# Kernel tuning notes

Hardware: AMD Instinct MI355X
Metric: run time of the kernel (lower is better)

The kernel has to match this reference:

```python
import jax, jax.numpy as jnp
import numpy as np

COMMITMENT_COST = 0.25


def setup_inputs() -> dict:
    key = jax.random.key(0)
    k1, k2 = jax.random.split(key)
    B, C, H, W, D = 8, 64, 32, 32, 32
    NUM_EMB = 512
    x = jax.random.normal(k1, (B, C, H, W, D), dtype=jnp.float32)
    # torch init: uniform(-1/num_embeddings, 1/num_embeddings)
    codebook = jax.random.uniform(k2, (NUM_EMB, C), dtype=jnp.float32,
                                  minval=-1.0 / NUM_EMB, maxval=1.0 / NUM_EMB)
    return {"x": x, "codebook": codebook}


def reference(x, codebook):
    B, C, H, W, D = x.shape
    # [B,C,H,W,D] -> [N, C] with N = B*H*W*D
    flat = jnp.transpose(x, (0, 2, 3, 4, 1)).reshape(-1, C)
    # squared L2 distances to every codebook entry: [N, num_embeddings]
    dist = (jnp.sum(flat * flat, axis=1, keepdims=True)
            - 2.0 * flat @ codebook.T
            + jnp.sum(codebook * codebook, axis=1))
    idx = jnp.argmin(dist, axis=1)                     # [N]
    # one-hot @ codebook  ==  gather (same math, efficient form)
    quant_flat = codebook[idx]                          # [N, C]
    quant = jnp.transpose(quant_flat.reshape(B, H, W, D, C), (0, 4, 1, 2, 3))
    e_loss = jnp.mean((jax.lax.stop_gradient(quant) - x) ** 2)
    q_loss = jnp.mean((quant - jax.lax.stop_gradient(x)) ** 2)
    loss = q_loss + COMMITMENT_COST * e_loss
    # straight-through estimator
    quant_st = x + jax.lax.stop_gradient(quant - x)
    return quant_st, loss
```

## Files before the change

kernel.cpp:

```cpp
#include <hip/hip_runtime.h>
#include <cstdint>
#include <cstddef>

#define SPATIAL   32768
#define CHANNELS  64
#define NUM_EMB   512
#define NPOS      262144
#define OUT_ELEMS 16777216
#define BLOCK     256
#define LOSS_SCALE (1.25f / 16777216.0f)

typedef __attribute__((ext_vector_type(8))) short bf16x8;
typedef __attribute__((ext_vector_type(4))) float f32x4;

union b8u { int i[4]; bf16x8 v; };
union fiu { float f; unsigned u; };

__device__ __forceinline__ short f2bf_rne(float f) {
    fiu v; v.f = f;
    unsigned r = v.u + 0x7fffu + ((v.u >> 16) & 1u);
    return (short)(r >> 16);
}

__global__ void vq_prep(const float* __restrict__ cb,
                        short* __restrict__ cbfrag,
                        float* __restrict__ cbn,
                        float* __restrict__ loss_slot) {
    int e = blockIdx.x * blockDim.x + threadIdx.x;
    if (e == 0) *loss_slot = 0.0f;
    if (e < NUM_EMB) {
        const int nt  = e >> 4;
        const int col = e & 15;
        float s = 0.0f;
#pragma unroll
        for (int q = 0; q < 4; ++q) {
#pragma unroll
            for (int j = 0; j < 8; ++j) {
                float v0 = cb[e * CHANNELS + q * 8 + j];
                float v1 = cb[e * CHANNELS + 32 + q * 8 + j];
                cbfrag[nt * 1024 + (q * 16 + col) * 8 + j]       = f2bf_rne(v0);
                cbfrag[nt * 1024 + 512 + (q * 16 + col) * 8 + j] = f2bf_rne(v1);
            }
        }
#pragma unroll
        for (int c = 0; c < CHANNELS; ++c) {
            float v = cb[e * CHANNELS + c];
            s = __builtin_fmaf(v, v, s);
        }
        cbn[e] = -0.5f * s;
    }
}

__global__ __launch_bounds__(BLOCK) void vq_main(
    const float* __restrict__ x,
    const float* __restrict__ cb,
    const short* __restrict__ cbfrag,
    const float* __restrict__ cbn,
    float* __restrict__ out,
    float* __restrict__ loss_slot) {
#pragma clang fp contract(off)
    __shared__ int   cand[BLOCK];
    __shared__ float wsum[4];

    const int tid  = threadIdx.x;
    const int wave = tid >> 6, lane = tid & 63;
    const int q    = lane >> 4, col = lane & 15;

    const int blockPos = blockIdx.x * BLOCK;
    const int b     = blockPos >> 15;
    const int sbase = blockPos & 32767;
    const float* xb = x + (size_t)b * (CHANNELS * SPATIAL);
    const int wbase = sbase + wave * 64;

    b8u A[4][2];
#pragma unroll
    for (int t = 0; t < 4; ++t) {
        const unsigned* pu = (const unsigned*)xb + (wbase + t * 16 + col);
#pragma unroll
        for (int kh = 0; kh < 2; ++kh) {
#pragma unroll
            for (int jj = 0; jj < 4; ++jj) {
                unsigned u0 = pu[(size_t)(kh * 32 + q * 8 + 2 * jj + 0) * SPATIAL];
                unsigned u1 = pu[(size_t)(kh * 32 + q * 8 + 2 * jj + 1) * SPATIAL];
                A[t][kh].i[jj] = __builtin_amdgcn_perm(u1, u0, 0x07060302u);
            }
        }
    }

    float m[4][4];
#pragma unroll
    for (int t = 0; t < 4; ++t)
#pragma unroll
        for (int r = 0; r < 4; ++r) m[t][r] = -3.4e38f;

    const unsigned MASK = 0xFFFFFE00u;
    const int encBase = 511 - col;

    for (int nt = 0; nt < 32; ++nt) {
        const int e0 = nt * 16;
        const short* fbase = cbfrag + nt * 1024 + lane * 8;
        bf16x8 B0 = *(const bf16x8*)(fbase);
        bf16x8 B1 = *(const bf16x8*)(fbase + 512);
        float cn = cbn[e0 + col];
        f32x4 ci = {cn, cn, cn, cn};
        const unsigned enc = (unsigned)(encBase - e0);
#pragma unroll
        for (int t = 0; t < 4; ++t) {
            f32x4 acc = __builtin_amdgcn_mfma_f32_16x16x32_bf16(A[t][0].v, B0, ci, 0, 0, 0);
            acc = __builtin_amdgcn_mfma_f32_16x16x32_bf16(A[t][1].v, B1, acc, 0, 0, 0);
#pragma unroll
            for (int r = 0; r < 4; ++r) {
                fiu p; p.f = acc[r];
                p.u = (p.u & MASK) | enc;
                m[t][r] = fmaxf(m[t][r], p.f);
            }
        }
    }

#pragma unroll
    for (int t = 0; t < 4; ++t) {
#pragma unroll
        for (int r = 0; r < 4; ++r) {
            float v = m[t][r];
#pragma unroll
            for (int d = 1; d < 16; d <<= 1)
                v = fmaxf(v, __shfl_xor(v, d, 64));
            if (col == 0) {
                fiu p; p.f = v;
                cand[wave * 64 + t * 16 + q * 4 + r] = 511 - (int)(p.u & 511u);
            }
        }
    }

    const int bidx = cand[tid];
    const f32x4* qv = (const f32x4*)(cb + (size_t)bidx * CHANNELS);
    const float* px = xb + (sbase + tid);
    float* op = out + (size_t)b * (CHANNELS * SPATIAL) + (sbase + tid);
    float lsum = 0.0f;
#pragma unroll
    for (int c4 = 0; c4 < 16; ++c4) {
        f32x4 qq = qv[c4];
#pragma unroll
        for (int j = 0; j < 4; ++j) {
            const int c = c4 * 4 + j;
            float xv = px[(size_t)c * SPATIAL];
            float t2 = qq[j] - xv;
            op[(size_t)c * SPATIAL] = xv + t2;
            lsum = __builtin_fmaf(t2, t2, lsum);
        }
    }

#pragma unroll
    for (int off = 32; off > 0; off >>= 1) lsum += __shfl_down(lsum, off, 64);
    if (lane == 0) wsum[wave] = lsum;
    __syncthreads();
    if (tid == 0) {
        float bs = (wsum[0] + wsum[1]) + (wsum[2] + wsum[3]);
        atomicAdd(loss_slot, bs * LOSS_SCALE);
    }
}

extern "C" void kernel_launch(void* const* d_in, const int* in_sizes, int n_in,
                              void* d_out, int out_size, void* d_ws, size_t ws_size,
                              hipStream_t stream) {
    const float* x  = (const float*)d_in[0];
    const float* cb = (const float*)d_in[1];
    float* out = (float*)d_out;
    short* cbfrag = (short*)d_ws;
    float* cbn    = (float*)(cbfrag + NUM_EMB * CHANNELS);
    float* loss_slot = out + OUT_ELEMS;

    vq_prep<<<2, 256, 0, stream>>>(cb, cbfrag, cbn, loss_slot);
    vq_main<<<NPOS / BLOCK, BLOCK, 0, stream>>>(x, cb, cbfrag, cbn, out, loss_slot);
}
```

Before: 149.2 us.

## Stage codebook fragments in LDS with double-buffered async loads and coalesced gather

The bf16 codebook fragments are now loaded into shared memory in four chunks using global_load_lds, double-buffered so the next chunk streams in while MFMAs run on the current one. The epilogue gather of selected codebook rows is restaged through a swizzled LDS buffer with coalesced row loads, in two halves of 32 channels. This is meant to cut per-wave global/L2 traffic for codebook reads and make the gather coalesced. The cost is 32KB of LDS per block, which may lower occupancy, plus extra barriers.

```diff
diff --git a/kernel.cpp b/kernel.cpp
--- a/kernel.cpp
+++ b/kernel.cpp
@@ -9,6 +9,11 @@
 #define OUT_ELEMS 16777216
 #define BLOCK     256
 #define LOSS_SCALE (1.25f / 16777216.0f)
+
+#define NT_TOTAL     32
+#define NT_PER_CHUNK 8
+#define NCHUNK       4
+#define CHUNK_BYTES  16384
 
 typedef __attribute__((ext_vector_type(8))) short bf16x8;
 typedef __attribute__((ext_vector_type(4))) float f32x4;
@@ -59,8 +64,12 @@
     float* __restrict__ out,
     float* __restrict__ loss_slot) {
 #pragma clang fp contract(off)
+    __shared__ __align__(16) char smem[32768];
     __shared__ int   cand[BLOCK];
     __shared__ float wsum[4];
+
+    short* stageS = (short*)smem;
+    float* qbuf   = (float*)smem;
 
     const int tid  = threadIdx.x;
     const int wave = tid >> 6, lane = tid & 63;
@@ -72,6 +81,18 @@
     const float* xb = x + (size_t)b * (CHANNELS * SPATIAL);
     const int wbase = sbase + wave * 64;
 
+    {
+#pragma unroll
+        for (int rd = 0; rd < 4; ++rd) {
+            const int off = rd * 4096 + wave * 1024;
+            const unsigned* g = (const unsigned*)((const char*)cbfrag + off + lane * 16);
+            unsigned* l = (unsigned*)(smem + off);
+            __builtin_amdgcn_global_load_lds(
+                (const __attribute__((address_space(1))) unsigned*)g,
+                (__attribute__((address_space(3))) unsigned*)l, 16, 0, 0);
+        }
+    }
+
     b8u A[4][2];
 #pragma unroll
     for (int t = 0; t < 4; ++t) {
@@ -96,25 +117,46 @@
     const unsigned MASK = 0xFFFFFE00u;
     const int encBase = 511 - col;
 
-    for (int nt = 0; nt < 32; ++nt) {
-        const int e0 = nt * 16;
-        const short* fbase = cbfrag + nt * 1024 + lane * 8;
-        bf16x8 B0 = *(const bf16x8*)(fbase);
-        bf16x8 B1 = *(const bf16x8*)(fbase + 512);
-        float cn = cbn[e0 + col];
-        f32x4 ci = {cn, cn, cn, cn};
-        const unsigned enc = (unsigned)(encBase - e0);
-#pragma unroll
-        for (int t = 0; t < 4; ++t) {
-            f32x4 acc = __builtin_amdgcn_mfma_f32_16x16x32_bf16(A[t][0].v, B0, ci, 0, 0, 0);
-            acc = __builtin_amdgcn_mfma_f32_16x16x32_bf16(A[t][1].v, B1, acc, 0, 0, 0);
-#pragma unroll
-            for (int r = 0; r < 4; ++r) {
-                fiu p; p.f = acc[r];
-                p.u = (p.u & MASK) | enc;
-                m[t][r] = fmaxf(m[t][r], p.f);
-            }
-        }
+    __syncthreads();
+
+#pragma unroll 1
+    for (int c = 0; c < NCHUNK; ++c) {
+        const int buf = c & 1;
+        if (c + 1 < NCHUNK) {
+#pragma unroll
+            for (int rd = 0; rd < 4; ++rd) {
+                const int off = rd * 4096 + wave * 1024;
+                const unsigned* g = (const unsigned*)
+                    ((const char*)cbfrag + (c + 1) * CHUNK_BYTES + off + lane * 16);
+                unsigned* l = (unsigned*)(smem + (buf ^ 1) * CHUNK_BYTES + off);
+                __builtin_amdgcn_global_load_lds(
+                    (const __attribute__((address_space(1))) unsigned*)g,
+                    (__attribute__((address_space(3))) unsigned*)l, 16, 0, 0);
+            }
+        }
+#pragma unroll
+        for (int k = 0; k < NT_PER_CHUNK; ++k) {
+            const int nt = c * NT_PER_CHUNK + k;
+            const int e0 = nt * 16;
+            const short* sb = stageS + buf * (CHUNK_BYTES / 2) + k * 1024 + lane * 8;
+            bf16x8 B0 = *(const bf16x8*)sb;
+            bf16x8 B1 = *(const bf16x8*)(sb + 512);
+            float cn = cbn[e0 + col];
+            f32x4 ci = {cn, cn, cn, cn};
+            const unsigned enc = (unsigned)(encBase - e0);
+#pragma unroll
+            for (int t = 0; t < 4; ++t) {
+                f32x4 acc = __builtin_amdgcn_mfma_f32_16x16x32_bf16(A[t][0].v, B0, ci, 0, 0, 0);
+                acc = __builtin_amdgcn_mfma_f32_16x16x32_bf16(A[t][1].v, B1, acc, 0, 0, 0);
+#pragma unroll
+                for (int r = 0; r < 4; ++r) {
+                    fiu p; p.f = acc[r];
+                    p.u = (p.u & MASK) | enc;
+                    m[t][r] = fmaxf(m[t][r], p.f);
+                }
+            }
+        }
+        __syncthreads();
     }
 
 #pragma unroll
@@ -131,23 +173,42 @@
             }
         }
     }
-
-    const int bidx = cand[tid];
-    const f32x4* qv = (const f32x4*)(cb + (size_t)bidx * CHANNELS);
-    const float* px = xb + (sbase + tid);
-    float* op = out + (size_t)b * (CHANNELS * SPATIAL) + (sbase + tid);
+    __syncthreads();
+
+    const int pos = tid;
+    const int gr  = tid >> 3;
+    const int gl  = tid & 7;
+    const float* pxb = xb + (sbase + pos);
+    float* opb = out + (size_t)b * (CHANNELS * SPATIAL) + (sbase + pos);
     float lsum = 0.0f;
-#pragma unroll
-    for (int c4 = 0; c4 < 16; ++c4) {
-        f32x4 qq = qv[c4];
-#pragma unroll
-        for (int j = 0; j < 4; ++j) {
-            const int c = c4 * 4 + j;
-            float xv = px[(size_t)c * SPATIAL];
-            float t2 = qq[j] - xv;
-            op[(size_t)c * SPATIAL] = xv + t2;
-            lsum = __builtin_fmaf(t2, t2, lsum);
-        }
+
+#pragma unroll 1
+    for (int cc = 0; cc < 2; ++cc) {
+#pragma unroll
+        for (int rd = 0; rd < 8; ++rd) {
+            const int r   = rd * 32 + gr;
+            const int row = cand[r];
+            f32x4 v = *((const f32x4*)(cb + (size_t)row * CHANNELS + cc * 32) + gl);
+            const int lsw = gl ^ (r & 7);
+            *((f32x4*)(qbuf + r * 32 + lsw * 4)) = v;
+        }
+        __syncthreads();
+        const float* px = pxb + (size_t)(cc * 32) * SPATIAL;
+        float* op = opb + (size_t)(cc * 32) * SPATIAL;
+#pragma unroll
+        for (int j = 0; j < 8; ++j) {
+            const int jsw = j ^ (pos & 7);
+            f32x4 qq = *((const f32x4*)(qbuf + pos * 32 + jsw * 4));
+#pragma unroll
+            for (int k = 0; k < 4; ++k) {
+                const int ch = j * 4 + k;
+                float xv = px[(size_t)ch * SPATIAL];
+                float t2 = qq[k] - xv;
+                op[(size_t)ch * SPATIAL] = xv + t2;
+                lsum = __builtin_fmaf(t2, t2, lsum);
+            }
+        }
+        if (cc == 0) __syncthreads();
     }
 
 #pragma unroll
```

Measured after the change: 141.6 us. 1.05x faster.

## Stage codebook fragments in LDS with double-buffered async loads and halve positions per block

Applied to the files above, without the earlier changes.

Each block now handles 128 positions instead of 256 with the same 256 threads, and swaps the MFMA operand order so the codebook is the A operand. Codebook bf16 fragments are streamed into LDS through double-buffered global_load_lds copies instead of per-wave global loads. The output gather stages selected codebook rows in a swizzled LDS buffer so each thread reads vectors, and the loss/writeback loop is split across two thread halves. This is meant to cut register pressure (launch bounds raised to 6 blocks/CU) and repeated global codebook reads, at the cost of more __syncthreads and twice as many blocks.

```diff
diff --git a/kernel.cpp b/kernel.cpp
--- a/kernel.cpp
+++ b/kernel.cpp
@@ -8,6 +8,7 @@
 #define NPOS      262144
 #define OUT_ELEMS 16777216
 #define BLOCK     256
+#define POSB      128
 #define LOSS_SCALE (1.25f / 16777216.0f)
 
 typedef __attribute__((ext_vector_type(8))) short bf16x8;
@@ -51,7 +52,7 @@
     }
 }
 
-__global__ __launch_bounds__(BLOCK) void vq_main(
+__global__ __launch_bounds__(BLOCK, 6) void vq_main(
     const float* __restrict__ x,
     const float* __restrict__ cb,
     const short* __restrict__ cbfrag,
@@ -59,95 +60,136 @@
     float* __restrict__ out,
     float* __restrict__ loss_slot) {
 #pragma clang fp contract(off)
-    __shared__ int   cand[BLOCK];
+    __shared__ __align__(16) char arena[16384];
+    __shared__ int   cand[POSB];
     __shared__ float wsum[4];
+
+    short* stageS = (short*)arena;
+    float* qbuf   = (float*)arena;
 
     const int tid  = threadIdx.x;
     const int wave = tid >> 6, lane = tid & 63;
     const int q    = lane >> 4, col = lane & 15;
 
-    const int blockPos = blockIdx.x * BLOCK;
+    const int blockPos = blockIdx.x * POSB;
     const int b     = blockPos >> 15;
     const int sbase = blockPos & 32767;
     const float* xb = x + (size_t)b * (CHANNELS * SPATIAL);
-    const int wbase = sbase + wave * 64;
-
-    b8u A[4][2];
-#pragma unroll
-    for (int t = 0; t < 4; ++t) {
+    const int wbase = sbase + wave * 32;
+
+#pragma unroll
+    for (int rd = 0; rd < 2; ++rd) {
+        const int off = rd * 4096 + wave * 1024;
+        __builtin_amdgcn_global_load_lds(
+            (const __attribute__((address_space(1))) unsigned*)
+                ((const char*)cbfrag + off + lane * 16),
+            (__attribute__((address_space(3))) unsigned*)(arena + off), 16, 0, 0);
+    }
+    __builtin_amdgcn_sched_barrier(0);
+
+    b8u A[2][2];
+#pragma unroll
+    for (int t = 0; t < 2; ++t) {
         const unsigned* pu = (const unsigned*)xb + (wbase + t * 16 + col);
 #pragma unroll
-        for (int kh = 0; kh < 2; ++kh) {
+        for (int kh = 0; kh < 2; ++kh)
 #pragma unroll
             for (int jj = 0; jj < 4; ++jj) {
                 unsigned u0 = pu[(size_t)(kh * 32 + q * 8 + 2 * jj + 0) * SPATIAL];
                 unsigned u1 = pu[(size_t)(kh * 32 + q * 8 + 2 * jj + 1) * SPATIAL];
                 A[t][kh].i[jj] = __builtin_amdgcn_perm(u1, u0, 0x07060302u);
             }
-        }
-    }
-
-    float m[4][4];
-#pragma unroll
-    for (int t = 0; t < 4; ++t)
-#pragma unroll
-        for (int r = 0; r < 4; ++r) m[t][r] = -3.4e38f;
-
+    }
+
+    __syncthreads();
+
+    float mt[2];
+    mt[0] = -3.4e38f; mt[1] = -3.4e38f;
     const unsigned MASK = 0xFFFFFE00u;
-    const int encBase = 511 - col;
-
-    for (int nt = 0; nt < 32; ++nt) {
-        const int e0 = nt * 16;
-        const short* fbase = cbfrag + nt * 1024 + lane * 8;
-        bf16x8 B0 = *(const bf16x8*)(fbase);
-        bf16x8 B1 = *(const bf16x8*)(fbase + 512);
-        float cn = cbn[e0 + col];
-        f32x4 ci = {cn, cn, cn, cn};
-        const unsigned enc = (unsigned)(encBase - e0);
-#pragma unroll
-        for (int t = 0; t < 4; ++t) {
-            f32x4 acc = __builtin_amdgcn_mfma_f32_16x16x32_bf16(A[t][0].v, B0, ci, 0, 0, 0);
-            acc = __builtin_amdgcn_mfma_f32_16x16x32_bf16(A[t][1].v, B1, acc, 0, 0, 0);
-#pragma unroll
-            for (int r = 0; r < 4; ++r) {
-                fiu p; p.f = acc[r];
-                p.u = (p.u & MASK) | enc;
-                m[t][r] = fmaxf(m[t][r], p.f);
-            }
-        }
-    }
-
-#pragma unroll
-    for (int t = 0; t < 4; ++t) {
-#pragma unroll
-        for (int r = 0; r < 4; ++r) {
-            float v = m[t][r];
-#pragma unroll
-            for (int d = 1; d < 16; d <<= 1)
-                v = fmaxf(v, __shfl_xor(v, d, 64));
-            if (col == 0) {
-                fiu p; p.f = v;
-                cand[wave * 64 + t * 16 + q * 4 + r] = 511 - (int)(p.u & 511u);
-            }
-        }
-    }
-
-    const int bidx = cand[tid];
-    const f32x4* qv = (const f32x4*)(cb + (size_t)bidx * CHANNELS);
-    const float* px = xb + (sbase + tid);
-    float* op = out + (size_t)b * (CHANNELS * SPATIAL) + (sbase + tid);
+
+    int buf = 0;
+#pragma unroll 1
+    for (int c = 0; c < 8; ++c) {
+        if (c < 7) {
+#pragma unroll
+            for (int rd = 0; rd < 2; ++rd) {
+                const int off = rd * 4096 + wave * 1024;
+                __builtin_amdgcn_global_load_lds(
+                    (const __attribute__((address_space(1))) unsigned*)
+                        ((const char*)cbfrag + (c + 1) * 8192 + off + lane * 16),
+                    (__attribute__((address_space(3))) unsigned*)
+                        (arena + (buf ^ 1) * 8192 + off), 16, 0, 0);
+            }
+        }
+#pragma unroll
+        for (int k = 0; k < 4; ++k) {
+            const int nt = c * 4 + k;
+            const short* sb = stageS + buf * 4096 + k * 1024 + (lane << 3);
+            bf16x8 CB0 = *(const bf16x8*)sb;
+            bf16x8 CB1 = *(const bf16x8*)(sb + 512);
+            f32x4 civ  = *(const f32x4*)(cbn + nt * 16 + (q << 2));
+            const unsigned encq = (unsigned)(511 - nt * 16 - (q << 2));
+#pragma unroll
+            for (int tt = 0; tt < 2; ++tt) {
+                f32x4 acc = __builtin_amdgcn_mfma_f32_16x16x32_bf16(CB0, A[tt][0].v, civ, 0, 0, 0);
+                acc = __builtin_amdgcn_mfma_f32_16x16x32_bf16(CB1, A[tt][1].v, acc, 0, 0, 0);
+                fiu p0, p1, p2, p3;
+                p0.f = acc[0]; p0.u = (p0.u & MASK) | (encq - 0);
+                p1.f = acc[1]; p1.u = (p1.u & MASK) | (encq - 1);
+                p2.f = acc[2]; p2.u = (p2.u & MASK) | (encq - 2);
+                p3.f = acc[3]; p3.u = (p3.u & MASK) | (encq - 3);
+                float mm = fmaxf(fmaxf(p0.f, p1.f), fmaxf(p2.f, p3.f));
+                mt[tt] = fmaxf(mt[tt], mm);
+            }
+        }
+        __syncthreads();
+        buf ^= 1;
+    }
+
+#pragma unroll
+    for (int t = 0; t < 2; ++t) {
+        float v = mt[t];
+        v = fmaxf(v, __shfl_xor(v, 16, 64));
+        v = fmaxf(v, __shfl_xor(v, 32, 64));
+        if (lane < 16) {
+            fiu p; p.f = v;
+            cand[wave * 32 + t * 16 + lane] = 511 - (int)(p.u & 511u);
+        }
+    }
+    __syncthreads();
+
+    const int pos = tid & (POSB - 1);
+    const int sub = tid >> 7;
+    const int gr  = tid >> 3;
+    const int gl  = tid & 7;
+    const float* pxb = xb + (sbase + pos);
+    float* opb = out + (size_t)b * (CHANNELS * SPATIAL) + (sbase + pos);
     float lsum = 0.0f;
-#pragma unroll
-    for (int c4 = 0; c4 < 16; ++c4) {
-        f32x4 qq = qv[c4];
+
+#pragma unroll 1
+    for (int cc = 0; cc < 2; ++cc) {
+#pragma unroll
+        for (int rd = 0; rd < 4; ++rd) {
+            const int r   = rd * 32 + gr;
+            const int row = cand[r];
+            f32x4 v = *((const f32x4*)(cb + (size_t)row * CHANNELS + cc * 32) + gl);
+            *((f32x4*)(qbuf + r * 32 + ((gl ^ (r & 7)) << 2))) = v;
+        }
+        __syncthreads();
 #pragma unroll
         for (int j = 0; j < 4; ++j) {
-            const int c = c4 * 4 + j;
-            float xv = px[(size_t)c * SPATIAL];
-            float t2 = qq[j] - xv;
-            op[(size_t)c * SPATIAL] = xv + t2;
-            lsum = __builtin_fmaf(t2, t2, lsum);
-        }
+            const int jj = sub * 4 + j;
+            f32x4 qq = *((const f32x4*)(qbuf + pos * 32 + ((jj ^ (pos & 7)) << 2)));
+#pragma unroll
+            for (int k = 0; k < 4; ++k) {
+                const int ch = cc * 32 + jj * 4 + k;
+                float xv = pxb[(size_t)ch * SPATIAL];
+                float t2 = qq[k] - xv;
+                opb[(size_t)ch * SPATIAL] = xv + t2;
+                lsum = __builtin_fmaf(t2, t2, lsum);
+            }
+        }
+        if (cc == 0) __syncthreads();
     }
 
 #pragma unroll
@@ -171,5 +213,5 @@
     float* loss_slot = out + OUT_ELEMS;
 
     vq_prep<<<2, 256, 0, stream>>>(cb, cbfrag, cbn, loss_slot);
-    vq_main<<<NPOS / BLOCK, BLOCK, 0, stream>>>(x, cb, cbfrag, cbn, out, loss_slot);
-}
+    vq_main<<<NPOS / POSB, BLOCK, 0, stream>>>(x, cb, cbfrag, cbn, out, loss_slot);
+}
```

Result: slower. 153.3 us (+2.7%).
